# Kernel tuning notes

Hardware: AMD Instinct MI355X
Metric: run time of the kernel (lower is better)

## Reference

```python
import jax, jax.numpy as jnp
import numpy as np

N = 16384
NUM_EMB = 8192
D = 512
K_SEL = 4
COMMIT = 0.25


def setup_inputs() -> dict:
    key = jax.random.key(0)
    k1, k2 = jax.random.split(key)
    z_e = jax.random.normal(k1, (N, D), dtype=jnp.float32)
    # torch init: uniform(-1/num_embeddings, 1/num_embeddings)
    lim = 1.0 / NUM_EMB
    codebook = jax.random.uniform(k2, (NUM_EMB, D), dtype=jnp.float32,
                                  minval=-lim, maxval=lim)
    return {"z_e": z_e, "codebook": codebook, "k": K_SEL}


def reference(z_e, codebook, k):
    # distances: ||z||^2 - 2 z.W^T + ||w||^2  -> [N, NUM_EMB]
    distances = (jnp.sum(z_e * z_e, axis=1, keepdims=True)
                 - 2.0 * jnp.matmul(z_e, codebook.T)
                 + jnp.sum(codebook * codebook, axis=1))
    # top-k smallest distances
    _, indices = jax.lax.top_k(-distances, k)  # [N, k]
    n = z_e.shape[0]
    k_hot = jnp.zeros((n, codebook.shape[0]), dtype=z_e.dtype)
    k_hot = k_hot.at[jnp.arange(n)[:, None], indices].set(1.0)
    quantized_k = codebook[indices]            # [N, k, D]
    z_q = quantized_k.mean(axis=1)             # [N, D]
    codebook_loss = jnp.mean((z_q - jax.lax.stop_gradient(z_e)) ** 2)
    commitment_loss = COMMIT * jnp.mean((z_e - jax.lax.stop_gradient(z_q)) ** 2)
    vq_loss = codebook_loss + commitment_loss
    z_q_ste = z_e + jax.lax.stop_gradient(z_q - z_e)  # straight-through
    return (z_q_ste, vq_loss, k_hot)
```

## Files before the change

kernel.cpp:

```cpp
#include <hip/hip_runtime.h>

#define N_ROWS 16384
#define N_EMB  8192
#define DIM    512
#define NCAND  16


typedef short  bhalf8  __attribute__((ext_vector_type(8)));
typedef float  floatx4 __attribute__((ext_vector_type(4)));

__device__ __forceinline__ unsigned short f2b(float f) {
    unsigned u = __builtin_bit_cast(unsigned, f);
    unsigned r = (u + 0x7fffu + ((u >> 16) & 1u)) >> 16;
    return (unsigned short)r;
}
__device__ __forceinline__ unsigned pk2(float a, float b) {
    return (unsigned)f2b(a) | ((unsigned)f2b(b) << 16);
}
__device__ __forceinline__ unsigned mkkey(float s, int col) {
    unsigned short b = f2b(s);
    unsigned short ts = (unsigned short)(b ^ ((b & 0x8000u) ? 0xFFFFu : 0x8000u));
    return ((unsigned)ts << 16) | (unsigned)col;
}
__device__ __forceinline__ unsigned umn(unsigned a, unsigned b) { return a < b ? a : b; }

__global__ void convert_bf16_kernel(const float* __restrict__ ze,
                                    const float* __restrict__ cb,
                                    unsigned short* __restrict__ ze16,
                                    unsigned short* __restrict__ cb16) {
    size_t id = (size_t)blockIdx.x * 256 + threadIdx.x;
    const size_t nze = (size_t)N_ROWS * DIM / 8;
    const float* src;
    unsigned short* dst;
    size_t off;
    if (id < nze) { src = ze; dst = ze16; off = id * 8; }
    else          { src = cb; dst = cb16; off = (id - nze) * 8; }
    float4 a = *(const float4*)(src + off);
    float4 b = *(const float4*)(src + off + 4);
    uint4 u = { pk2(a.x, a.y), pk2(a.z, a.w), pk2(b.x, b.y), pk2(b.z, b.w) };
    *(uint4*)(dst + off) = u;
}

__launch_bounds__(256, 3)
__global__ void score_gemm_topk_kernel(const unsigned short* __restrict__ ze16,
                                       const unsigned short* __restrict__ cb16,
                                       unsigned* __restrict__ blkTop) {
    __shared__ unsigned short As[128][40];
    __shared__ unsigned short Bs[128][40];

    const int t    = threadIdx.x;
    const int lane = t & 63;
    const int w    = t >> 6;
    const int rowBase = blockIdx.y * 128;
    const int colBase = blockIdx.x * 128;
    const int cblk    = blockIdx.x;

    const int m = lane & 15;
    const int q = lane >> 4;

    floatx4 acc[2][8];
    #pragma unroll
    for (int i = 0; i < 2; ++i)
        #pragma unroll
        for (int j = 0; j < 8; ++j)
            acc[i][j] = (floatx4){0.0f, 0.0f, 0.0f, 0.0f};

    const int sr = t >> 1;
    const int sk = (t & 1) * 16;
    const unsigned short* pa = ze16 + (size_t)(rowBase + sr) * DIM + sk;
    const unsigned short* pb = cb16 + (size_t)(colBase + sr) * DIM + sk;

    for (int k0 = 0; k0 < DIM; k0 += 32) {
        uint4 va0 = *(const uint4*)(pa + k0);
        uint4 va1 = *(const uint4*)(pa + k0 + 8);
        uint4 vb0 = *(const uint4*)(pb + k0);
        uint4 vb1 = *(const uint4*)(pb + k0 + 8);
        __syncthreads();
        *(uint4*)&As[sr][sk]     = va0;
        *(uint4*)&As[sr][sk + 8] = va1;
        *(uint4*)&Bs[sr][sk]     = vb0;
        *(uint4*)&Bs[sr][sk + 8] = vb1;
        __syncthreads();

        bhalf8 af0 = *(bhalf8*)&As[w * 32 + m][q * 8];
        bhalf8 af1 = *(bhalf8*)&As[w * 32 + 16 + m][q * 8];
        #pragma unroll
        for (int j = 0; j < 8; ++j) {
            bhalf8 bf = *(bhalf8*)&Bs[j * 16 + m][q * 8];
            acc[0][j] = __builtin_amdgcn_mfma_f32_16x16x32_bf16(af0, bf, acc[0][j], 0, 0, 0);
            acc[1][j] = __builtin_amdgcn_mfma_f32_16x16x32_bf16(af1, bf, acc[1][j], 0, 0, 0);
        }
    }

    #pragma unroll
    for (int i = 0; i < 2; ++i) {
        #pragma unroll
        for (int reg = 0; reg < 4; ++reg) {
            const int grow = rowBase + w * 32 + i * 16 + q * 4 + reg;
            unsigned kk[8];
            #pragma unroll
            for (int j = 0; j < 8; ++j) {
                unsigned e = mkkey(-acc[i][j][reg], colBase + j * 16 + m);
                kk[j] = e;
                #pragma unroll
                for (int s = 7; s > 0; --s) {
                    if (s <= j) {
                        unsigned lo = umn(kk[s - 1], kk[s]);
                        unsigned hi = kk[s - 1] < kk[s] ? kk[s] : kk[s - 1];
                        kk[s - 1] = lo; kk[s] = hi;
                    }
                }
            }
            unsigned sval = 0;
            #pragma unroll
            for (int s = 0; s < 8; ++s) {
                unsigned g = kk[0];
                g = umn(g, (unsigned)__shfl_xor((int)g, 1, 64));
                g = umn(g, (unsigned)__shfl_xor((int)g, 2, 64));
                g = umn(g, (unsigned)__shfl_xor((int)g, 4, 64));
                g = umn(g, (unsigned)__shfl_xor((int)g, 8, 64));
                bool pop = (kk[0] == g);
                #pragma unroll
                for (int u = 0; u < 7; ++u) kk[u] = pop ? kk[u + 1] : kk[u];
                kk[7] = pop ? 0xFFFFFFFFu : kk[7];
                sval = (m == s) ? g : sval;
            }
            if (m < 8)
                blkTop[((size_t)grow * 64 + cblk) * 8 + m] = sval;
        }
    }
}

__global__ void merge_topk_kernel(const unsigned* __restrict__ blkTop,
                                  int* __restrict__ cand) {
    const int wv   = threadIdx.x >> 6;
    const int lane = threadIdx.x & 63;
    const int row  = blockIdx.x * 4 + wv;
    const uint4* base = (const uint4*)(blkTop + (size_t)row * 512);

    uint4 a = base[lane * 2];
    uint4 b = base[lane * 2 + 1];
    unsigned in[8] = { a.x, a.y, a.z, a.w, b.x, b.y, b.z, b.w };
    unsigned kk[8];
    #pragma unroll
    for (int j = 0; j < 8; ++j) {
        kk[j] = in[j];
        #pragma unroll
        for (int s = 7; s > 0; --s) {
            if (s <= j) {
                unsigned lo = umn(kk[s - 1], kk[s]);
                unsigned hi = kk[s - 1] < kk[s] ? kk[s] : kk[s - 1];
                kk[s - 1] = lo; kk[s] = hi;
            }
        }
    }

    unsigned sval = 0;
    #pragma unroll
    for (int s = 0; s < NCAND; ++s) {
        unsigned g = kk[0];
        #pragma unroll
        for (int d = 32; d; d >>= 1)
            g = umn(g, (unsigned)__shfl_xor((int)g, d, 64));
        bool pop = (kk[0] == g);
        #pragma unroll
        for (int u = 0; u < 7; ++u) kk[u] = pop ? kk[u + 1] : kk[u];
        kk[7] = pop ? 0xFFFFFFFFu : kk[7];
        sval = (lane == s) ? g : sval;
    }
    if (lane < NCAND)
        cand[(size_t)row * NCAND + lane] = (int)(sval & 0xFFFFu);
}

__global__ void rescore_kernel(const float* __restrict__ ze,
                               const float* __restrict__ cb,
                               const int* __restrict__ cand,
                               float* __restrict__ out_zq,
                               float* __restrict__ out_khot,
                               double* __restrict__ lossAcc) {
    __shared__ float zsh[4][DIM];
    const int wv = threadIdx.x >> 6;
    const int lane = threadIdx.x & 63;
    const int row = blockIdx.x * 4 + wv;

    {
        const float* zp = ze + (size_t)row * DIM + lane * 8;
        float4 v0 = *(const float4*)zp;
        float4 v1 = *(const float4*)(zp + 4);
        *(float4*)&zsh[wv][lane * 8]     = v0;
        *(float4*)&zsh[wv][lane * 8 + 4] = v1;
    }
    __syncthreads();

    float racc = 0.0f;
    {
        const int b = (lane >> 3) & 3;
        const int j = lane & 7;
        const float* zr = &zsh[wv][128 * b + j];
        #pragma unroll
        for (int i = 0; i < 16; ++i) {
            float zk = zr[8 * i];
            float sq = zk * zk;
            asm volatile("" : "+v"(sq));
            racc = racc + sq;
        }
    }
    float t1 = racc + __shfl_xor(racc, 1, 64);
    float t2 = t1 + __shfl_xor(t1, 2, 64);
    float t3 = t2 + __shfl_xor(t2, 4, 64);
    float zn = (__shfl(t3, 0, 64) + __shfl(t3, 8, 64))
             + (__shfl(t3, 16, 64) + __shfl(t3, 24, 64));

    float qv = 3.0e38f;
    int   idxv = 0x7fffffff;
    if (lane < NCAND) {
        idxv = cand[(size_t)row * NCAND + lane];
        const float* wp = cb + (size_t)idxv * DIM;
        const float* zz = zsh[wv];
        float acc1 = 0.0f;
        for (int k = 0; k < 384; k += 8) {
            float4 wa = *(const float4*)(wp + k);
            float4 wb = *(const float4*)(wp + k + 4);
            acc1 = __builtin_fmaf(zz[k + 0], wa.x, acc1);
            acc1 = __builtin_fmaf(zz[k + 1], wa.y, acc1);
            acc1 = __builtin_fmaf(zz[k + 2], wa.z, acc1);
            acc1 = __builtin_fmaf(zz[k + 3], wa.w, acc1);
            acc1 = __builtin_fmaf(zz[k + 4], wb.x, acc1);
            acc1 = __builtin_fmaf(zz[k + 5], wb.y, acc1);
            acc1 = __builtin_fmaf(zz[k + 6], wb.z, acc1);
            acc1 = __builtin_fmaf(zz[k + 7], wb.w, acc1);
        }
        float acc2 = 0.0f;
        for (int k = 384; k < 512; k += 8) {
            float4 wa = *(const float4*)(wp + k);
            float4 wb = *(const float4*)(wp + k + 4);
            acc2 = __builtin_fmaf(zz[k + 0], wa.x, acc2);
            acc2 = __builtin_fmaf(zz[k + 1], wa.y, acc2);
            acc2 = __builtin_fmaf(zz[k + 2], wa.z, acc2);
            acc2 = __builtin_fmaf(zz[k + 3], wa.w, acc2);
            acc2 = __builtin_fmaf(zz[k + 4], wb.x, acc2);
            acc2 = __builtin_fmaf(zz[k + 5], wb.y, acc2);
            acc2 = __builtin_fmaf(zz[k + 6], wb.z, acc2);
            acc2 = __builtin_fmaf(zz[k + 7], wb.w, acc2);
        }
        float Cv = acc1 + acc2;
        qv = zn - 2.0f * Cv;
    }

    float q[NCAND]; int id[NCAND];
    #pragma unroll
    for (int c = 0; c < NCAND; ++c) {
        q[c]  = __shfl(qv, c, 64);
        id[c] = __shfl(idxv, c, 64);
    }
    int selIdx[4];
    bool used[NCAND];
    #pragma unroll
    for (int c = 0; c < NCAND; ++c) used[c] = false;
    #pragma unroll
    for (int s = 0; s < 4; ++s) {
        float bq = 3.0e38f; int bi = 0x7fffffff; int bc = -1;
        #pragma unroll
        for (int c = 0; c < NCAND; ++c) {
            bool better = !used[c] && (q[c] < bq || (q[c] == bq && id[c] < bi));
            if (better) { bq = q[c]; bi = id[c]; bc = c; }
        }
        selIdx[s] = bi;
        #pragma unroll
        for (int c = 0; c < NCAND; ++c) used[c] = used[c] || (c == bc);
    }

    float zq[8] = { 0, 0, 0, 0, 0, 0, 0, 0 };
    #pragma unroll
    for (int s = 0; s < 4; ++s) {
        const float* wp = cb + (size_t)selIdx[s] * DIM + lane * 8;
        float4 w0 = *(const float4*)wp;
        float4 w1 = *(const float4*)(wp + 4);
        zq[0] += w0.x; zq[1] += w0.y; zq[2] += w0.z; zq[3] += w0.w;
        zq[4] += w1.x; zq[5] += w1.y; zq[6] += w1.z; zq[7] += w1.w;
    }

    float zf[8];
    {
        const float* zz = &zsh[wv][lane * 8];
        #pragma unroll
        for (int i = 0; i < 8; ++i) zf[i] = zz[i];
    }
    float o[8];
    double l = 0.0;
    #pragma unroll
    for (int i = 0; i < 8; ++i) {
        float zqf  = zq[i] * 0.25f;
        float diff = zqf - zf[i];
        o[i] = zf[i] + diff;
        double ld = (double)diff;
        l += ld * ld;
    }
    {
        float* op = out_zq + (size_t)row * DIM + lane * 8;
        float4 v0 = { o[0], o[1], o[2], o[3] };
        float4 v1 = { o[4], o[5], o[6], o[7] };
        *(float4*)op = v0;
        *(float4*)(op + 4) = v1;
    }
    #pragma unroll
    for (int mm = 32; mm; mm >>= 1) l += __shfl_xor(l, mm, 64);
    if (lane == 0) atomicAdd(lossAcc, l);

    if (lane < 4)
        out_khot[(size_t)row * N_EMB + selIdx[lane]] = 1.0f;
}

__global__ void finalize_kernel(const double* __restrict__ lossAcc,
                                float* __restrict__ out_loss) {
    if (threadIdx.x == 0 && blockIdx.x == 0)
        out_loss[0] = (float)(lossAcc[0] * (1.25 / ((double)N_ROWS * (double)DIM)));
}

extern "C" void kernel_launch(void* const* d_in, const int* in_sizes, int n_in,
                              void* d_out, int out_size, void* d_ws, size_t ws_size,
                              hipStream_t stream) {
    (void)in_sizes; (void)n_in; (void)out_size; (void)ws_size;
    const float* ze = (const float*)d_in[0];
    const float* cb = (const float*)d_in[1];

    float* out      = (float*)d_out;
    float* out_zq   = out;
    float* out_loss = out + (size_t)N_ROWS * DIM;
    float* out_khot = out_loss + 1;

    double* lossAcc = (double*)d_ws;
    int*    cand    = (int*)((char*)d_ws + 16);

    char* base = (char*)d_out;
    unsigned*       blkTop = (unsigned*)(base + 33554448);
    unsigned short* ze16   = (unsigned short*)(base + 33554448 + 33554432);
    unsigned short* cb16   = ze16 + (size_t)N_ROWS * DIM;

    hipMemsetAsync(lossAcc, 0, 16, stream);

    convert_bf16_kernel<<<6144, 256, 0, stream>>>(ze, cb, ze16, cb16);
    score_gemm_topk_kernel<<<dim3(N_EMB / 128, N_ROWS / 128), 256, 0, stream>>>(ze16, cb16, blkTop);
    merge_topk_kernel<<<N_ROWS / 4, 256, 0, stream>>>(blkTop, cand);
    hipMemsetAsync(out_khot, 0, (size_t)N_ROWS * N_EMB * sizeof(float), stream);
    rescore_kernel<<<N_ROWS / 4, 256, 0, stream>>>(ze, cb, cand, out_zq, out_khot, lossAcc);
    finalize_kernel<<<1, 64, 0, stream>>>(lossAcc, out_loss);
}
```

Measured before the change: 1.117 ms.

## Use direct global-to-LDS loads with swizzle in GEMM, fuse k-hot zeroing into rescore

The score GEMM now stages A and B tiles with global_load_lds straight into an XOR-swizzled shared layout, using a K step of 64 instead of 32. This removes the register round-trip and halves the number of barrier pairs. Separately, the rescore kernel writes the entire k-hot row itself, zeros and ones, with vectorized float4 stores, which replaces the 512MB memset plus scattered ones. The costs are a larger shared-memory footprint and more store logic per row.

```diff
diff --git a/kernel.cpp b/kernel.cpp
--- a/kernel.cpp
+++ b/kernel.cpp
@@ -4,6 +4,9 @@
 #define N_EMB  8192
 #define DIM    512
 #define NCAND  16
+
+#define GAS __attribute__((address_space(1)))
+#define LAS __attribute__((address_space(3)))
 
 
 typedef short  bhalf8  __attribute__((ext_vector_type(8)));
@@ -45,8 +48,8 @@
 __global__ void score_gemm_topk_kernel(const unsigned short* __restrict__ ze16,
                                        const unsigned short* __restrict__ cb16,
                                        unsigned* __restrict__ blkTop) {
-    __shared__ unsigned short As[128][40];
-    __shared__ unsigned short Bs[128][40];
+    __shared__ unsigned short Amm[128 * 64];
+    __shared__ unsigned short Bmm[128 * 64];
 
     const int t    = threadIdx.x;
     const int lane = t & 63;
@@ -65,30 +68,37 @@
         for (int j = 0; j < 8; ++j)
             acc[i][j] = (floatx4){0.0f, 0.0f, 0.0f, 0.0f};
 
-    const int sr = t >> 1;
-    const int sk = (t & 1) * 16;
-    const unsigned short* pa = ze16 + (size_t)(rowBase + sr) * DIM + sk;
-    const unsigned short* pb = cb16 + (size_t)(colBase + sr) * DIM + sk;
-
-    for (int k0 = 0; k0 < DIM; k0 += 32) {
-        uint4 va0 = *(const uint4*)(pa + k0);
-        uint4 va1 = *(const uint4*)(pa + k0 + 8);
-        uint4 vb0 = *(const uint4*)(pb + k0);
-        uint4 vb1 = *(const uint4*)(pb + k0 + 8);
+    const int tr = t >> 3;
+    const int cg = (t & 7) ^ (tr & 7);
+    const unsigned short* pa = ze16 + (size_t)(rowBase + tr) * DIM + cg * 8;
+    const unsigned short* pb = cb16 + (size_t)(colBase + tr) * DIM + cg * 8;
+
+    const int ch0 = ((0 * 4 + q) ^ (m & 7)) * 8;
+    const int ch1 = ((1 * 4 + q) ^ (m & 7)) * 8;
+
+    for (int k0 = 0; k0 < DIM; k0 += 64) {
         __syncthreads();
-        *(uint4*)&As[sr][sk]     = va0;
-        *(uint4*)&As[sr][sk + 8] = va1;
-        *(uint4*)&Bs[sr][sk]     = vb0;
-        *(uint4*)&Bs[sr][sk + 8] = vb1;
+        #pragma unroll
+        for (int k = 0; k < 4; ++k)
+            __builtin_amdgcn_global_load_lds((const GAS void*)(pa + (size_t)k * 32 * DIM + k0),
+                                             (LAS void*)(Amm + (k * 256 + w * 64) * 8), 16, 0, 0);
+        #pragma unroll
+        for (int k = 0; k < 4; ++k)
+            __builtin_amdgcn_global_load_lds((const GAS void*)(pb + (size_t)k * 32 * DIM + k0),
+                                             (LAS void*)(Bmm + (k * 256 + w * 64) * 8), 16, 0, 0);
         __syncthreads();
 
-        bhalf8 af0 = *(bhalf8*)&As[w * 32 + m][q * 8];
-        bhalf8 af1 = *(bhalf8*)&As[w * 32 + 16 + m][q * 8];
-        #pragma unroll
-        for (int j = 0; j < 8; ++j) {
-            bhalf8 bf = *(bhalf8*)&Bs[j * 16 + m][q * 8];
-            acc[0][j] = __builtin_amdgcn_mfma_f32_16x16x32_bf16(af0, bf, acc[0][j], 0, 0, 0);
-            acc[1][j] = __builtin_amdgcn_mfma_f32_16x16x32_bf16(af1, bf, acc[1][j], 0, 0, 0);
+        #pragma unroll
+        for (int h = 0; h < 2; ++h) {
+            const int ch = h ? ch1 : ch0;
+            bhalf8 af0 = *(bhalf8*)&Amm[(w * 32 + m) * 64 + ch];
+            bhalf8 af1 = *(bhalf8*)&Amm[(w * 32 + 16 + m) * 64 + ch];
+            #pragma unroll
+            for (int j = 0; j < 8; ++j) {
+                bhalf8 bf = *(bhalf8*)&Bmm[(j * 16 + m) * 64 + ch];
+                acc[0][j] = __builtin_amdgcn_mfma_f32_16x16x32_bf16(af0, bf, acc[0][j], 0, 0, 0);
+                acc[1][j] = __builtin_amdgcn_mfma_f32_16x16x32_bf16(af1, bf, acc[1][j], 0, 0, 0);
+            }
         }
     }
 
@@ -307,8 +317,29 @@
     for (int mm = 32; mm; mm >>= 1) l += __shfl_xor(l, mm, 64);
     if (lane == 0) atomicAdd(lossAcc, l);
 
-    if (lane < 4)
-        out_khot[(size_t)row * N_EMB + selIdx[lane]] = 1.0f;
+    unsigned hotm[4] = { 0u, 0u, 0u, 0u };
+    #pragma unroll
+    for (int s = 0; s < 4; ++s) {
+        int si = selIdx[s];
+        bool own = ((si >> 2) & 63) == lane;
+        int jj = si >> 8;
+        unsigned bit = 1u << (((jj & 7) << 2) | (si & 3));
+        int word = jj >> 3;
+        #pragma unroll
+        for (int wd = 0; wd < 4; ++wd)
+            hotm[wd] |= (own && word == wd) ? bit : 0u;
+    }
+    float* kp = out_khot + (size_t)row * N_EMB;
+    #pragma unroll
+    for (int j = 0; j < 32; ++j) {
+        unsigned bits = (hotm[j >> 3] >> ((j & 7) * 4)) & 0xFu;
+        float4 v;
+        v.x = (bits & 1u) ? 1.0f : 0.0f;
+        v.y = (bits & 2u) ? 1.0f : 0.0f;
+        v.z = (bits & 4u) ? 1.0f : 0.0f;
+        v.w = (bits & 8u) ? 1.0f : 0.0f;
+        *(float4*)(kp + j * 256 + lane * 4) = v;
+    }
 }
 
 __global__ void finalize_kernel(const double* __restrict__ lossAcc,
@@ -342,7 +373,6 @@
     convert_bf16_kernel<<<6144, 256, 0, stream>>>(ze, cb, ze16, cb16);
     score_gemm_topk_kernel<<<dim3(N_EMB / 128, N_ROWS / 128), 256, 0, stream>>>(ze16, cb16, blkTop);
     merge_topk_kernel<<<N_ROWS / 4, 256, 0, stream>>>(blkTop, cand);
-    hipMemsetAsync(out_khot, 0, (size_t)N_ROWS * N_EMB * sizeof(float), stream);
     rescore_kernel<<<N_ROWS / 4, 256, 0, stream>>>(ze, cb, cand, out_zq, out_khot, lossAcc);
     finalize_kernel<<<1, 64, 0, stream>>>(lossAcc, out_loss);
 }
```

New measurement: 1.017 ms. 9.0% less time.
